# Optimization experiments

Measured on AMD Instinct MI355X. Metric: run time of the kernel, lower is better.

Reference implementation:

```python
import jax, jax.numpy as jnp
import numpy as np
from functools import partial

D = 1024
H = 4 * D
E = 8
K_TOP = 2
B, T = 4, 2048
NEG_INF = jnp.float32(-1e30)


def setup_inputs() -> dict:
    key = jax.random.key(0)
    ks = jax.random.split(key, 12)
    s = 0.02
    return {
        "x": jax.random.normal(ks[0], (B, T, D), jnp.float32),
        "noise": jax.random.normal(ks[1], (B, T, E), jnp.float32),
        "gate_w": jax.random.normal(ks[2], (E, D), jnp.float32) * s,
        "gate_b": jnp.zeros((E,), jnp.float32),
        "var_w": jax.random.normal(ks[3], (E, D), jnp.float32) * s,
        "var_b": jnp.zeros((E,), jnp.float32),
        "w1": jax.random.normal(ks[4], (E, H, D), jnp.float32) * s,
        "b1": jnp.zeros((E, H), jnp.float32),
        "w2": jax.random.normal(ks[5], (E, D, H), jnp.float32) * s,
        "b2": jnp.zeros((E, D), jnp.float32),
    }


def reference(x, noise, gate_w, gate_b, var_w, var_b, w1, b1, w2, b2):
    # Noisy top-k gating
    logits = jnp.einsum("btd,ed->bte", x, gate_w) + gate_b          # [B,T,E]
    std = jax.nn.softplus(jnp.einsum("btd,ed->bte", x, var_w) + var_b)
    noisy = logits + noise * std                                      # [B,T,E]
    _, idx = jax.lax.top_k(noisy, K_TOP)                              # [B,T,K]
    # boolean top-k mask over experts
    mask = (idx[..., None] == jnp.arange(E)).any(axis=-2)             # [B,T,E]
    coef = jax.nn.softmax(jnp.where(mask, noisy, NEG_INF), axis=-1)   # zeros outside top-k

    # Combine: sum_e coef_e * FFN_e(x). coef is exactly 0 for non-selected
    # experts, so this equals the masked gather/scatter math. Scan over the
    # small expert dim to avoid a [E,B,T,H] intermediate.
    coef_e = jnp.moveaxis(coef, -1, 0)                                # [E,B,T]

    def body(acc, ew):
        w1e, b1e, w2e, b2e, ce = ew
        h = jax.nn.relu(jnp.einsum("btd,hd->bth", x, w1e) + b1e)
        y = jnp.einsum("bth,dh->btd", h, w2e) + b2e
        return acc + y * ce[..., None], None

    out, _ = jax.lax.scan(body, jnp.zeros_like(x), (w1, b1, w2, b2, coef_e))
    return out
```

## Files before the change

kernel.cpp:

```cpp
#include <hip/hip_runtime.h>
#include <hip/hip_bf16.h>
#include <math.h>

#define NTOK 8192
#define DD   1024
#define HH   4096
#define NE   8
#define BM 128
#define BN 128
#define BK 64
#define SLOT_CAP (2 * NTOK + NE * BM)

typedef __bf16 bf16;
typedef __bf16 bf16x8 __attribute__((ext_vector_type(8)));
typedef __bf16 bf16x4 __attribute__((ext_vector_type(4)));
typedef float  f32x4  __attribute__((ext_vector_type(4)));

typedef __attribute__((address_space(3))) unsigned char lds_u8;
typedef const __attribute__((address_space(1))) unsigned char g_u8;

__device__ __forceinline__ void gload16(const bf16* g, bf16* l) {
  __builtin_amdgcn_global_load_lds((g_u8*)g, (lds_u8*)l, 16, 0, 0);
}

__device__ __forceinline__ float softplus_f(float v) {
  return fmaxf(v, 0.f) + log1pf(expf(-fabsf(v)));
}

__global__ __launch_bounds__(64) void moe_gate_kernel(
    const float* __restrict__ x, const float* __restrict__ noise,
    const float* __restrict__ gate_w, const float* __restrict__ gate_b,
    const float* __restrict__ var_w,  const float* __restrict__ var_b,
    float* __restrict__ coef2, int* __restrict__ t2e, int* __restrict__ counts,
    bf16* __restrict__ xb)
{
  const int lane = threadIdx.x;
  const float4* gw4 = (const float4*)gate_w;
  const float4* vw4 = (const float4*)var_w;
  for (int tt = 0; tt < 16; ++tt) {
    const int t = blockIdx.x * 16 + tt;
    const float4* x4 = (const float4*)(x + (size_t)t * DD);
    bf16x4* xb4 = (bf16x4*)(xb + (size_t)t * DD);
    float pg[NE], pv[NE];
    #pragma unroll
    for (int e = 0; e < NE; ++e) { pg[e] = 0.f; pv[e] = 0.f; }
    #pragma unroll
    for (int i = 0; i < DD / 256; ++i) {
      const int d4 = i * 64 + lane;
      const float4 f = x4[d4];
      bf16x4 v;
      v[0] = (bf16)f.x; v[1] = (bf16)f.y; v[2] = (bf16)f.z; v[3] = (bf16)f.w;
      xb4[d4] = v;
      #pragma unroll
      for (int e = 0; e < NE; ++e) {
        const float4 g = gw4[e * 256 + d4];
        pg[e] = fmaf(f.x, g.x, fmaf(f.y, g.y, fmaf(f.z, g.z, fmaf(f.w, g.w, pg[e]))));
        const float4 w = vw4[e * 256 + d4];
        pv[e] = fmaf(f.x, w.x, fmaf(f.y, w.y, fmaf(f.z, w.z, fmaf(f.w, w.w, pv[e]))));
      }
    }
    #pragma unroll
    for (int e = 0; e < NE; ++e) {
      #pragma unroll
      for (int off = 32; off; off >>= 1) {
        pg[e] += __shfl_xor(pg[e], off);
        pv[e] += __shfl_xor(pv[e], off);
      }
    }
    if (lane == 0) {
      float noisy[NE];
      #pragma unroll
      for (int e = 0; e < NE; ++e) {
        const float lg = pg[e] + gate_b[e];
        const float sd = softplus_f(pv[e] + var_b[e]);
        noisy[e] = lg + noise[t * NE + e] * sd;
      }
      int i1 = 0; float n1 = noisy[0];
      #pragma unroll
      for (int e = 1; e < NE; ++e) if (noisy[e] > n1) { n1 = noisy[e]; i1 = e; }
      int i2 = -1; float n2 = -3.0e38f;
      #pragma unroll
      for (int e = 0; e < NE; ++e) if (e != i1 && noisy[e] > n2) { n2 = noisy[e]; i2 = e; }
      const float e2 = expf(n2 - n1);
      const float den = 1.f + e2;
      coef2[t * 2 + 0] = 1.f / den;
      coef2[t * 2 + 1] = e2 / den;
      t2e[t * 2 + 0] = i1;
      t2e[t * 2 + 1] = i2;
      atomicAdd(&counts[i1], 1);
      atomicAdd(&counts[i2], 1);
    }
  }
}

__global__ void moe_offsets_kernel(const int* __restrict__ counts, int* __restrict__ po) {
  if (threadIdx.x == 0) {
    int acc = 0;
    po[0] = 0;
    for (int e = 0; e < NE; ++e) {
      acc += ((counts[e] + BM - 1) / BM) * BM;
      po[e + 1] = acc;
    }
  }
}

__global__ __launch_bounds__(256) void moe_scatter_kernel(
    const int* __restrict__ t2e, const float* __restrict__ coef2,
    const int* __restrict__ po, int* __restrict__ cnt2,
    int* __restrict__ assign_tok, float* __restrict__ slot_coef)
{
  const int t = blockIdx.x * 256 + threadIdx.x;
  if (t >= NTOK) return;
  #pragma unroll
  for (int k = 0; k < 2; ++k) {
    const int e = t2e[t * 2 + k];
    const int pos = atomicAdd(&cnt2[e], 1);
    const int slot = po[e] + pos;
    assign_tok[slot] = t;
    slot_coef[slot] = coef2[t * 2 + k];
  }
}

__global__ __launch_bounds__(256) void cvt2_bf16_kernel(
    const float* __restrict__ s1, bf16* __restrict__ d1, int n41,
    const float* __restrict__ s2, bf16* __restrict__ d2, int n42)
{
  for (int i = blockIdx.x * 256 + threadIdx.x; i < n41 + n42; i += gridDim.x * 256) {
    const float* s = (i < n41) ? s1 : s2;
    bf16* d = (i < n41) ? d1 : d2;
    const int j = (i < n41) ? i : i - n41;
    const float4 f = ((const float4*)s)[j];
    bf16x4 v;
    v[0] = (bf16)f.x; v[1] = (bf16)f.y; v[2] = (bf16)f.z; v[3] = (bf16)f.w;
    ((bf16x4*)d)[j] = v;
  }
}

template<int KDIM, int NCOLS, bool FFN1>
__global__ __launch_bounds__(256) void moe_gemm_kernel(
    const bf16* __restrict__ Asrc, const bf16* __restrict__ Wsrc,
    const float* __restrict__ bias,
    const int* __restrict__ assign_tok, const float* __restrict__ slot_coef,
    const int* __restrict__ po,
    bf16* __restrict__ hout, float* __restrict__ out,
    int chunk_base, int gx)
{
  __shared__ bf16 As[BM][BK];
  __shared__ bf16 Bs[BN][BK];
  __shared__ int toks[BM];

  const int nwg = gridDim.x;
  const int lin = blockIdx.x;
  const int q = nwg >> 3, r = nwg & 7;
  const int xcd = lin & 7, idx = lin >> 3;
  const int wg = (xcd < r ? xcd * (q + 1) : r * (q + 1) + (xcd - r) * q) + idx;
  int bx, by;
  if constexpr (FFN1) { bx = wg % gx; by = wg / gx; }
  else               { by = wg % (NCOLS / BN); bx = wg / (NCOLS / BN); }

  const int po8 = po[NE];
  const int row0 = chunk_base + bx * BM;
  if (row0 >= po8) return;
  int e = 0;
  while (row0 >= po[e + 1]) ++e;
  const int bn0 = by * BN;
  const bf16* We = Wsrc + (size_t)e * ((size_t)HH * DD);
  const int tid = threadIdx.x, lane = tid & 63, wave = tid >> 6;
  if (tid < BM) toks[tid] = assign_tok[row0 + tid];
  __syncthreads();

  const int rin = lane >> 3;
  const int c8s = (lane & 7) * 8;
  const bf16* asrc[4];
  const bf16* bsrc[4];
  #pragma unroll
  for (int i = 0; i < 4; ++i) {
    const int row = (wave * 4 + i) * 8 + rin;
    int ar;
    if constexpr (FFN1) {
      const int s = toks[row];
      ar = s < 0 ? 0 : s;
    } else {
      ar = row0 - chunk_base + row;
    }
    asrc[i] = Asrc + (size_t)ar * KDIM + c8s;
    bsrc[i] = We + (size_t)(bn0 + row) * KDIM + c8s;
  }

  const int la = lane & 15, hi = lane >> 4;
  const int wm = (wave >> 1) * 64, wn = (wave & 1) * 64;
  f32x4 acc[4][4];
  #pragma unroll
  for (int m = 0; m < 4; ++m)
    #pragma unroll
    for (int n = 0; n < 4; ++n) acc[m][n] = {0.f, 0.f, 0.f, 0.f};

  for (int k0 = 0; k0 < KDIM; k0 += BK) {
    #pragma unroll
    for (int i = 0; i < 4; ++i) gload16(asrc[i] + k0, &As[(wave * 4 + i) * 8][0]);
    #pragma unroll
    for (int i = 0; i < 4; ++i) gload16(bsrc[i] + k0, &Bs[(wave * 4 + i) * 8][0]);
    __syncthreads();
    #pragma unroll
    for (int ks = 0; ks < 2; ++ks) {
      bf16x8 af[4], bff[4];
      #pragma unroll
      for (int m = 0; m < 4; ++m)
        af[m] = *(const bf16x8*)(&As[wm + m * 16 + la][ks * 32 + hi * 8]);
      #pragma unroll
      for (int n = 0; n < 4; ++n)
        bff[n] = *(const bf16x8*)(&Bs[wn + n * 16 + la][ks * 32 + hi * 8]);
      #pragma unroll
      for (int m = 0; m < 4; ++m)
        #pragma unroll
        for (int n = 0; n < 4; ++n)
          acc[m][n] = __builtin_amdgcn_mfma_f32_16x16x32_bf16(af[m], bff[n], acc[m][n], 0, 0, 0);
    }
    __syncthreads();
  }

  if constexpr (FFN1) {
    const int hrow0 = row0 - chunk_base;
    #pragma unroll
    for (int n = 0; n < 4; ++n) {
      const int col = bn0 + wn + n * 16 + la;
      const float bb = bias[e * NCOLS + col];
      #pragma unroll
      for (int m = 0; m < 4; ++m) {
        const int rbase = wm + m * 16 + hi * 4;
        #pragma unroll
        for (int rr = 0; rr < 4; ++rr) {
          float v = acc[m][n][rr] + bb;
          v = v > 0.f ? v : 0.f;
          hout[(size_t)(hrow0 + rbase + rr) * HH + col] = (bf16)v;
        }
      }
    }
  } else {
    #pragma unroll
    for (int n = 0; n < 4; ++n) {
      const int col = bn0 + wn + n * 16 + la;
      const float bb = bias[e * NCOLS + col];
      #pragma unroll
      for (int m = 0; m < 4; ++m) {
        const int rbase = wm + m * 16 + hi * 4;
        #pragma unroll
        for (int rr = 0; rr < 4; ++rr) {
          const int trow = rbase + rr;
          const int tok = toks[trow];
          if (tok >= 0) {
            const float c = slot_coef[row0 + trow];
            atomicAdd(out + (size_t)tok * DD + col, c * (acc[m][n][rr] + bb));
          }
        }
      }
    }
  }
}

extern "C" void kernel_launch(void* const* d_in, const int* in_sizes, int n_in,
                              void* d_out, int out_size, void* d_ws, size_t ws_size,
                              hipStream_t stream) {
  const float* x      = (const float*)d_in[0];
  const float* noise  = (const float*)d_in[1];
  const float* gate_w = (const float*)d_in[2];
  const float* gate_b = (const float*)d_in[3];
  const float* var_w  = (const float*)d_in[4];
  const float* var_b  = (const float*)d_in[5];
  const float* w1     = (const float*)d_in[6];
  const float* b1     = (const float*)d_in[7];
  const float* w2     = (const float*)d_in[8];
  const float* b2     = (const float*)d_in[9];
  float* out = (float*)d_out;
  (void)in_sizes; (void)n_in; (void)out_size;

  char* ws = (char*)d_ws;
  size_t off = 0;
  auto alloc = [&](size_t bytes) {
    off = (off + 255) & ~(size_t)255;
    size_t o = off;
    off += bytes;
    return o;
  };
  bf16*  xb         = (bf16*)(ws + alloc((size_t)NTOK * DD * 2));
  float* coef2      = (float*)(ws + alloc((size_t)NTOK * 2 * 4));
  int*   t2e        = (int*)(ws + alloc((size_t)NTOK * 2 * 4));
  int*   counts     = (int*)(ws + alloc(64));
  int*   cnt2       = counts + 8;
  int*   po         = (int*)(ws + alloc(64));
  int*   assign_tok = (int*)(ws + alloc((size_t)SLOT_CAP * 4));
  float* slot_coef  = (float*)(ws + alloc((size_t)SLOT_CAP * 4));
  bf16*  w1b        = (bf16*)(ws + alloc((size_t)NE * HH * DD * 2));
  bf16*  w2b        = (bf16*)(ws + alloc((size_t)NE * DD * HH * 2));
  off = (off + 255) & ~(size_t)255;
  const size_t h_avail = ws_size > off ? ws_size - off : 0;
  int chunk_rows = (int)(h_avail / ((size_t)HH * 2));
  chunk_rows = (chunk_rows / BM) * BM;
  if (chunk_rows < BM) chunk_rows = BM;
  if (chunk_rows > SLOT_CAP) chunk_rows = SLOT_CAP;
  bf16* hbuf = (bf16*)(ws + off);

  hipMemsetAsync(counts, 0, 64, stream);
  hipMemsetAsync(assign_tok, 0xFF, (size_t)SLOT_CAP * 4, stream);
  hipMemsetAsync(out, 0, (size_t)NTOK * DD * 4, stream);

  moe_gate_kernel<<<NTOK / 16, 64, 0, stream>>>(x, noise, gate_w, gate_b, var_w, var_b,
                                                coef2, t2e, counts, xb);
  moe_offsets_kernel<<<1, 64, 0, stream>>>(counts, po);
  moe_scatter_kernel<<<NTOK / 256, 256, 0, stream>>>(t2e, coef2, po, cnt2,
                                                     assign_tok, slot_coef);
  cvt2_bf16_kernel<<<2048, 256, 0, stream>>>(w1, w1b, NE * HH * DD / 4,
                                             w2, w2b, NE * DD * HH / 4);

  const int rounds = (SLOT_CAP + chunk_rows - 1) / chunk_rows;
  for (int r = 0; r < rounds; ++r) {
    const int cb = r * chunk_rows;
    const int rows_here = (cb + chunk_rows <= SLOT_CAP) ? chunk_rows : (SLOT_CAP - cb);
    const int gx = rows_here / BM;
    moe_gemm_kernel<DD, HH, true><<<gx * (HH / BN), 256, 0, stream>>>(
        xb, w1b, b1, assign_tok, slot_coef, po, hbuf, nullptr, cb, gx);
    moe_gemm_kernel<HH, DD, false><<<gx * (DD / BN), 256, 0, stream>>>(
        hbuf, w2b, b2, assign_tok, slot_coef, po, nullptr, out, cb, gx);
  }
}
```

Before: 1.008 ms.

## Fuse gate and weight conversion kernels and XOR-swizzle GEMM LDS tiles

Merges the gating kernel and the fp32-to-bf16 weight conversion into one launch. Extra blocks handle the conversion while the gate blocks now run four waves per block. Separately, the GEMM's LDS tiles use an XOR swizzle on 16-byte column chunks, applied both on the global-to-LDS load and on the fragment reads, to reduce LDS bank conflicts. The fused launch saves one kernel launch and lets the gate and conversion work overlap. The tail of the gate kernel (wave/lane reductions, counts) is not shown and must work with the new 256-thread layout.

```diff
diff --git a/kernel.cpp b/kernel.cpp
--- a/kernel.cpp
+++ b/kernel.cpp
@@ -10,6 +10,8 @@
 #define BN 128
 #define BK 64
 #define SLOT_CAP (2 * NTOK + NE * BM)
+#define GATE_BLOCKS 512
+#define CVT_BLOCKS  2048
 
 typedef __bf16 bf16;
 typedef __bf16 bf16x8 __attribute__((ext_vector_type(8)));
@@ -27,18 +29,35 @@
   return fmaxf(v, 0.f) + log1pf(expf(-fabsf(v)));
 }
 
-__global__ __launch_bounds__(64) void moe_gate_kernel(
+__global__ __launch_bounds__(256) void moe_gate_cvt_kernel(
     const float* __restrict__ x, const float* __restrict__ noise,
     const float* __restrict__ gate_w, const float* __restrict__ gate_b,
     const float* __restrict__ var_w,  const float* __restrict__ var_b,
     float* __restrict__ coef2, int* __restrict__ t2e, int* __restrict__ counts,
-    bf16* __restrict__ xb)
+    bf16* __restrict__ xb,
+    const float* __restrict__ w1, bf16* __restrict__ w1b, int n41,
+    const float* __restrict__ w2, bf16* __restrict__ w2b, int n42)
 {
-  const int lane = threadIdx.x;
+  if (blockIdx.x >= GATE_BLOCKS) {
+    const int i0 = (blockIdx.x - GATE_BLOCKS) * 256 + threadIdx.x;
+    const int stride = CVT_BLOCKS * 256;
+    for (int i = i0; i < n41 + n42; i += stride) {
+      const float* s = (i < n41) ? w1 : w2;
+      bf16* d = (i < n41) ? w1b : w2b;
+      const int j = (i < n41) ? i : i - n41;
+      const float4 f = ((const float4*)s)[j];
+      bf16x4 v;
+      v[0] = (bf16)f.x; v[1] = (bf16)f.y; v[2] = (bf16)f.z; v[3] = (bf16)f.w;
+      ((bf16x4*)d)[j] = v;
+    }
+    return;
+  }
+  const int lane = threadIdx.x & 63;
+  const int wave = threadIdx.x >> 6;
   const float4* gw4 = (const float4*)gate_w;
   const float4* vw4 = (const float4*)var_w;
-  for (int tt = 0; tt < 16; ++tt) {
-    const int t = blockIdx.x * 16 + tt;
+  for (int tt = 0; tt < 4; ++tt) {
+    const int t = blockIdx.x * 16 + wave * 4 + tt;
     const float4* x4 = (const float4*)(x + (size_t)t * DD);
     bf16x4* xb4 = (bf16x4*)(xb + (size_t)t * DD);
     float pg[NE], pv[NE];
@@ -121,21 +140,6 @@
   }
 }
 
-__global__ __launch_bounds__(256) void cvt2_bf16_kernel(
-    const float* __restrict__ s1, bf16* __restrict__ d1, int n41,
-    const float* __restrict__ s2, bf16* __restrict__ d2, int n42)
-{
-  for (int i = blockIdx.x * 256 + threadIdx.x; i < n41 + n42; i += gridDim.x * 256) {
-    const float* s = (i < n41) ? s1 : s2;
-    bf16* d = (i < n41) ? d1 : d2;
-    const int j = (i < n41) ? i : i - n41;
-    const float4 f = ((const float4*)s)[j];
-    bf16x4 v;
-    v[0] = (bf16)f.x; v[1] = (bf16)f.y; v[2] = (bf16)f.z; v[3] = (bf16)f.w;
-    ((bf16x4*)d)[j] = v;
-  }
-}
-
 template<int KDIM, int NCOLS, bool FFN1>
 __global__ __launch_bounds__(256) void moe_gemm_kernel(
     const bf16* __restrict__ Asrc, const bf16* __restrict__ Wsrc,
@@ -170,12 +174,13 @@
   __syncthreads();
 
   const int rin = lane >> 3;
-  const int c8s = (lane & 7) * 8;
+  const int c8s = ((lane & 7) ^ rin) * 8;
   const bf16* asrc[4];
   const bf16* bsrc[4];
   #pragma unroll
   for (int i = 0; i < 4; ++i) {
-    const int row = (wave * 4 + i) * 8 + rin;
+    const int c = wave * 4 + i;
+    const int row = c * 8 + rin;
     int ar;
     if constexpr (FFN1) {
       const int s = toks[row];
@@ -205,11 +210,17 @@
     for (int ks = 0; ks < 2; ++ks) {
       bf16x8 af[4], bff[4];
       #pragma unroll
-      for (int m = 0; m < 4; ++m)
-        af[m] = *(const bf16x8*)(&As[wm + m * 16 + la][ks * 32 + hi * 8]);
-      #pragma unroll
-      for (int n = 0; n < 4; ++n)
-        bff[n] = *(const bf16x8*)(&Bs[wn + n * 16 + la][ks * 32 + hi * 8]);
+      for (int m = 0; m < 4; ++m) {
+        const int row = wm + m * 16 + la;
+        const int c8 = (ks * 4 + hi) ^ (row & 7);
+        af[m] = *(const bf16x8*)(&As[row][c8 * 8]);
+      }
+      #pragma unroll
+      for (int n = 0; n < 4; ++n) {
+        const int row = wn + n * 16 + la;
+        const int c8 = (ks * 4 + hi) ^ (row & 7);
+        bff[n] = *(const bf16x8*)(&Bs[row][c8 * 8]);
+      }
       #pragma unroll
       for (int m = 0; m < 4; ++m)
         #pragma unroll
@@ -304,13 +315,12 @@
   hipMemsetAsync(assign_tok, 0xFF, (size_t)SLOT_CAP * 4, stream);
   hipMemsetAsync(out, 0, (size_t)NTOK * DD * 4, stream);
 
-  moe_gate_kernel<<<NTOK / 16, 64, 0, stream>>>(x, noise, gate_w, gate_b, var_w, var_b,
-                                                coef2, t2e, counts, xb);
+  moe_gate_cvt_kernel<<<GATE_BLOCKS + CVT_BLOCKS, 256, 0, stream>>>(
+      x, noise, gate_w, gate_b, var_w, var_b, coef2, t2e, counts, xb,
+      w1, w1b, NE * HH * DD / 4, w2, w2b, NE * DD * HH / 4);
   moe_offsets_kernel<<<1, 64, 0, stream>>>(counts, po);
   moe_scatter_kernel<<<NTOK / 256, 256, 0, stream>>>(t2e, coef2, po, cnt2,
                                                      assign_tok, slot_coef);
-  cvt2_bf16_kernel<<<2048, 256, 0, stream>>>(w1, w1b, NE * HH * DD / 4,
-                                             w2, w2b, NE * DD * HH / 4);
 
   const int rounds = (SLOT_CAP + chunk_rows - 1) / chunk_rows;
   for (int r = 0; r < rounds; ++r) {
```

New measurement: 999.0 us. About the same (-0.9%).
